# Kernel tuning notes

Measured on AMD Instinct MI355X. Metric: run time of the kernel, lower is better.

## Reference

```python
import jax, jax.numpy as jnp
import numpy as np

B, N, D = 4, 2048, 512   # batch, seq, feed_forward_size
H, DK, DV = 8, 64, 64    # heads, key_dim, value_dim
LN_EPS = 1e-5


def setup_inputs() -> dict:
    key = jax.random.key(0)
    ks = jax.random.split(key, 12)
    s = 0.02
    x = jax.random.normal(ks[0], (B, N, D), dtype=jnp.float32)
    # boolean mask, True = masked out (torch masked_fill semantics); causal
    attn_mask = ~jnp.tril(jnp.ones((N, N), dtype=bool))[None, None]
    ln_g = jnp.ones((D,), jnp.float32)
    ln_b = jnp.zeros((D,), jnp.float32)
    wq = jax.random.normal(ks[1], (D, H * DK), jnp.float32) * s
    bq = jnp.zeros((H * DK,), jnp.float32)
    wk = jax.random.normal(ks[2], (D, H * DK), jnp.float32) * s
    bk = jnp.zeros((H * DK,), jnp.float32)
    wv = jax.random.normal(ks[3], (D, H * DV), jnp.float32) * s
    bv = jnp.zeros((H * DV,), jnp.float32)
    wo = jax.random.normal(ks[4], (H * DV, D), jnp.float32) * s
    bo = jnp.zeros((D,), jnp.float32)
    return {"x": x, "attn_mask": attn_mask, "ln_g": ln_g, "ln_b": ln_b,
            "wq": wq, "bq": bq, "wk": wk, "bk": bk, "wv": wv, "bv": bv,
            "wo": wo, "bo": bo}


def _layernorm(x, g, b):
    mu = jnp.mean(x, axis=-1, keepdims=True)
    var = jnp.mean(jnp.square(x - mu), axis=-1, keepdims=True)
    return (x - mu) * jax.lax.rsqrt(var + LN_EPS) * g + b


def reference(x, attn_mask, ln_g, ln_b, wq, bq, wk, bk, wv, bv, wo, bo):
    xn = _layernorm(x, ln_g, ln_b)
    scale = DK ** -0.5
    q = (xn @ wq + bq).reshape(B, N, H, DK).transpose(0, 2, 1, 3) * scale  # b h n d
    k = (xn @ wk + bk).reshape(B, N, H, DK).transpose(0, 2, 1, 3)
    v = (xn @ wv + bv).reshape(B, N, H, DV).transpose(0, 2, 1, 3)
    sim = jnp.einsum('bhid,bhjd->bhij', q, k)
    sim = jnp.where(attn_mask, -jnp.finfo(sim.dtype).max, sim)
    attn = jax.nn.softmax(sim, axis=-1)  # dropout p=0 (eval)
    out = jnp.einsum('bhij,bhjd->bhid', attn, v)
    out = out.transpose(0, 2, 1, 3).reshape(B, N, H * DV)  # b n (h d)
    return out @ wo + bo
```

## Files before the change

kernel.cpp:

```cpp
#include <hip/hip_runtime.h>

typedef unsigned short u16;
typedef unsigned long long u64;
typedef __bf16 bf16x8 __attribute__((ext_vector_type(8)));
typedef float f32x4 __attribute__((ext_vector_type(4)));
typedef float f32x16 __attribute__((ext_vector_type(16)));

#define H_HEADS 8
#define DHEAD 64
#define NSEQ 2048
#define DMODEL 512
#define BATCH 4
#define MROWS (BATCH * NSEQ)
#define BH (BATCH * H_HEADS)

__device__ __forceinline__ u16 f2bf(float f) {
  unsigned u = __builtin_bit_cast(unsigned, f);
  u += 0x7fffu + ((u >> 16) & 1u);
  return (u16)(u >> 16);
}

__device__ __forceinline__ bf16x8 ldfrag(const u16* p) {
  return __builtin_bit_cast(bf16x8, *(const uint4*)p);
}

typedef __attribute__((address_space(1))) void GV;
typedef __attribute__((address_space(3))) void LV;
__device__ __forceinline__ void gld16(const void* g, void* l) {
  __builtin_amdgcn_global_load_lds((GV*)g, (LV*)l, 16, 0, 0);
}

__global__ __launch_bounds__(256) void ln_kernel(
    const float* __restrict__ x, const float* __restrict__ g,
    const float* __restrict__ b, u16* __restrict__ xn) {
  const int row = blockIdx.x;
  const int t = threadIdx.x;
  const float2 v = *(const float2*)(x + (size_t)row * DMODEL + t * 2);
  float s = v.x + v.y;
  float ss = v.x * v.x + v.y * v.y;
  #pragma unroll
  for (int d = 1; d < 64; d <<= 1) {
    s += __shfl_xor(s, d);
    ss += __shfl_xor(ss, d);
  }
  __shared__ float red[8];
  const int wave = t >> 6, lane = t & 63;
  if (lane == 0) { red[wave] = s; red[4 + wave] = ss; }
  __syncthreads();
  s = red[0] + red[1] + red[2] + red[3];
  ss = red[4] + red[5] + red[6] + red[7];
  const float mean = s * (1.0f / DMODEL);
  const float var = ss * (1.0f / DMODEL) - mean * mean;
  const float rstd = rsqrtf(var + 1e-5f);
  const float2 gg = *(const float2*)(g + t * 2);
  const float2 bb = *(const float2*)(b + t * 2);
  const float o0 = (v.x - mean) * rstd * gg.x + bb.x;
  const float o1 = (v.y - mean) * rstd * gg.y + bb.y;
  const unsigned packed = (unsigned)f2bf(o0) | ((unsigned)f2bf(o1) << 16);
  *(unsigned*)(xn + (size_t)row * DMODEL + t * 2) = packed;
}

__global__ __launch_bounds__(256) void transpose_w4_kernel(
    const float* __restrict__ w0, const float* __restrict__ w1,
    const float* __restrict__ w2, const float* __restrict__ w3,
    u16* __restrict__ WT) {
  __shared__ float tile[32][33];
  const int z = blockIdx.z;
  const float* W = (z == 0) ? w0 : (z == 1) ? w1 : (z == 2) ? w2 : w3;
  u16* dst = WT + (size_t)z * DMODEL * DMODEL;
  const int n0 = blockIdx.x * 32, k0 = blockIdx.y * 32;
  const int t = threadIdx.x;
  #pragma unroll
  for (int p = 0; p < 4; ++p) {
    const int u = p * 256 + t;
    const int r = u >> 5, c = u & 31;
    tile[r][c] = W[(size_t)(k0 + r) * DMODEL + n0 + c];
  }
  __syncthreads();
  #pragma unroll
  for (int p = 0; p < 4; ++p) {
    const int u = p * 256 + t;
    const int rn = u >> 5, ck = u & 31;
    dst[(size_t)(n0 + rn) * DMODEL + k0 + ck] = f2bf(tile[ck][rn]);
  }
}

template <int MODE>
__global__ __launch_bounds__(512) void gemm128_kernel(
    const u16* __restrict__ A, const u16* __restrict__ BT,
    const float* __restrict__ bq, const float* __restrict__ bk,
    const float* __restrict__ bv,
    u16* __restrict__ qb, u16* __restrict__ kb, u16* __restrict__ vtb,
    float* __restrict__ fout, int K) {
  __shared__ u16 lds_a[128 * 64];
  __shared__ u16 lds_b[128 * 64];
  const int t = threadIdx.x;
  const int lane = t & 63, wave = t >> 6;
  const int wm = wave >> 2, wn = wave & 3;
  const int lo = lane & 15, hi = lane >> 4;
  const int nwg = gridDim.x * gridDim.y;
  const int lid = blockIdx.y * gridDim.x + blockIdx.x;
  const int sid = (lid & 7) * (nwg >> 3) + (lid >> 3);
  const int m0 = (sid / gridDim.x) * 128, n0 = (sid % gridDim.x) * 128;
  const int sr = lane >> 3;
  const int scol = (((lane & 7) ^ sr) * 8);
  f32x4 acc[4][2] = {};
  for (int k0 = 0; k0 < K; k0 += 64) {
    #pragma unroll
    for (int j = 0; j < 2; ++j) {
      const int ch = wave * 2 + j;
      gld16(A + (size_t)(m0 + ch * 8 + sr) * K + k0 + scol, lds_a + ch * 512);
      gld16(BT + (size_t)(n0 + ch * 8 + sr) * K + k0 + scol, lds_b + ch * 512);
    }
    __syncthreads();
    #pragma unroll
    for (int kc = 0; kc < 2; ++kc) {
      bf16x8 af[4], bfr[2];
      const int sw = ((lo & 7) * 8);
      #pragma unroll
      for (int i = 0; i < 4; ++i)
        af[i] = ldfrag(lds_a + (wm * 64 + i * 16 + lo) * 64 + ((kc * 32 + hi * 8) ^ sw));
      #pragma unroll
      for (int i = 0; i < 2; ++i)
        bfr[i] = ldfrag(lds_b + (wn * 32 + i * 16 + lo) * 64 + ((kc * 32 + hi * 8) ^ sw));
      __builtin_amdgcn_s_setprio(1);
      #pragma unroll
      for (int mi = 0; mi < 4; ++mi)
        #pragma unroll
        for (int ni = 0; ni < 2; ++ni)
          acc[mi][ni] = __builtin_amdgcn_mfma_f32_16x16x32_bf16(
              af[mi], bfr[ni], acc[mi][ni], 0, 0, 0);
      __builtin_amdgcn_s_setprio(0);
    }
    __syncthreads();
  }
  #pragma unroll
  for (int mi = 0; mi < 4; ++mi) {
    #pragma unroll
    for (int ni = 0; ni < 2; ++ni) {
      const int col = n0 + wn * 32 + ni * 16 + lo;
      if (MODE == 0) {
        const int mat = col >> 9, w = col & 511;
        const int hh = w >> 6, dk = w & 63;
        const float bi = (mat == 0 ? bq : (mat == 1 ? bk : bv))[w];
        const int row0 = m0 + wm * 64 + mi * 16 + hi * 4;
        const int bbx = row0 >> 11, seq0 = row0 & 2047;
        if (mat == 2) {
          u64 pk = 0;
          #pragma unroll
          for (int r = 0; r < 4; ++r)
            pk |= (u64)f2bf(acc[mi][ni][r] + bi) << (16 * r);
          *(u64*)(vtb + ((size_t)(bbx * H_HEADS + hh) * DHEAD + dk) * NSEQ + seq0) = pk;
        } else {
          const float sc = (mat == 0) ? 0.18033688f : 1.0f;
          u16* dst = (mat == 0 ? qb : kb);
          #pragma unroll
          for (int r = 0; r < 4; ++r)
            dst[(((size_t)(bbx * H_HEADS + hh) * NSEQ) + seq0 + r) * DHEAD + dk] =
                f2bf((acc[mi][ni][r] + bi) * sc);
        }
      } else {
        const float bi = bq[col];
        #pragma unroll
        for (int r = 0; r < 4; ++r) {
          const int row = m0 + wm * 64 + mi * 16 + hi * 4 + r;
          fout[(size_t)row * DMODEL + col] = acc[mi][ni][r] + bi;
        }
      }
    }
  }
}

__global__ __launch_bounds__(256, 4) void attn_kernel(
    const u16* __restrict__ Q, const u16* __restrict__ K,
    const u16* __restrict__ VT, u16* __restrict__ O,
    float* __restrict__ pO, float* __restrict__ pML) {
  __shared__ u16 lds_k[2][4096];
  __shared__ u16 lds_v[2][4096];
  const int t = threadIdx.x;
  const int lane = t & 63, wave = t >> 6;
  const int l31 = lane & 31, hi = lane >> 5;
  const int l7 = lane & 7;

  const int nraw = blockIdx.x;
  const int n = (nraw & 7) * 160 + (nraw >> 3);
  const int bh = n / 40;
  const int r = n % 40;
  int qt, ck, C;
  if (r < 4)       { qt = r;                 C = 1; ck = 0; }
  else if (r < 12) { qt = 4 + ((r - 4) >> 1);  C = 2; ck = (r - 4) & 1; }
  else if (r < 24) { qt = 8 + (r - 12) / 3;    C = 3; ck = (r - 12) % 3; }
  else             { qt = 12 + ((r - 24) >> 2); C = 4; ck = (r - 24) & 3; }
  const int T = 2 * qt + 2;
  const int kc0 = ck * 8;
  const int L = min(8, T - kc0);

  const int b = bh >> 3, h = bh & 7;
  const u16* Qh = Q + (size_t)bh * NSEQ * DHEAD;
  const u16* Kh = K + (size_t)bh * NSEQ * DHEAD;
  const u16* Vh = VT + (size_t)bh * DHEAD * NSEQ;

  const int q0w = qt * 128 + wave * 32;
  const int lastkt = (q0w + 31) >> 6;
  const int qrow = q0w + l31;

  bf16x8 qf[4];
  #pragma unroll
  for (int c = 0; c < 4; ++c)
    qf[c] = ldfrag(Qh + (size_t)qrow * DHEAD + c * 16 + hi * 8);

  f32x16 o0 = {}, o1 = {};
  float m = -INFINITY, l = 0.0f;

  const int sr = lane >> 3;
  const int scol = ((lane & 7) ^ sr) * 8;
  const int swz = l7 * 8;

  #pragma unroll
  for (int j = 0; j < 2; ++j) {
    const int ch = wave * 2 + j;
    gld16(Kh + (size_t)(kc0 * 64 + ch * 8 + sr) * DHEAD + scol, lds_k[0] + ch * 512);
    gld16(Vh + (size_t)(ch * 8 + sr) * NSEQ + kc0 * 64 + scol, lds_v[0] + ch * 512);
  }

  for (int lt = 0; lt < L; ++lt) {
    const int gk = kc0 + lt;
    const int cur = lt & 1;
    if (lt + 1 < L) {
      const int kvn = (gk + 1) * 64;
      #pragma unroll
      for (int j = 0; j < 2; ++j) {
        const int ch = wave * 2 + j;
        gld16(Kh + (size_t)(kvn + ch * 8 + sr) * DHEAD + scol, lds_k[cur ^ 1] + ch * 512);
        gld16(Vh + (size_t)(ch * 8 + sr) * NSEQ + kvn + scol, lds_v[cur ^ 1] + ch * 512);
      }
      asm volatile("s_waitcnt vmcnt(4)" ::: "memory");
    } else {
      asm volatile("s_waitcnt vmcnt(0)" ::: "memory");
    }
    __builtin_amdgcn_s_barrier();
    __builtin_amdgcn_sched_barrier(0);

    if (gk <= lastkt) {
      const u16* lk = lds_k[cur];
      const u16* lv = lds_v[cur];
      f32x16 st0 = {}, st1 = {};

      __builtin_amdgcn_s_setprio(1);
      #pragma unroll
      for (int c = 0; c < 4; ++c) {
        const int col = (c * 16 + hi * 8) ^ swz;
        bf16x8 kf0 = ldfrag(lk + l31 * 64 + col);
        bf16x8 kf1 = ldfrag(lk + (32 + l31) * 64 + col);
        st0 = __builtin_amdgcn_mfma_f32_32x32x16_bf16(kf0, qf[c], st0, 0, 0, 0);
        st1 = __builtin_amdgcn_mfma_f32_32x32x16_bf16(kf1, qf[c], st1, 0, 0, 0);
      }
      __builtin_amdgcn_s_setprio(0);

      if (gk == lastkt) {
        const int kvb = gk * 64 + 4 * hi;
        #pragma unroll
        for (int rr = 0; rr < 16; ++rr) {
          const int kv = kvb + (rr & 3) + 8 * (rr >> 2);
          if (kv > qrow) st0[rr] = -1e30f;
          if (kv + 32 > qrow) st1[rr] = -1e30f;
        }
      }

      float mx[16];
      #pragma unroll
      for (int i = 0; i < 16; ++i) mx[i] = fmaxf(st0[i], st1[i]);
      #pragma unroll
      for (int stp = 8; stp; stp >>= 1)
        #pragma unroll
        for (int i = 0; i < stp; ++i) mx[i] = fmaxf(mx[i], mx[i + stp]);
      float pm = fmaxf(mx[0], __shfl_xor(mx[0], 32));

      if (__any(pm > m + 8.0f)) {
        const float mn = fmaxf(m, pm);
        const float sc = exp2f(m - mn);
        m = mn;
        l *= sc;
        #pragma unroll
        for (int rr = 0; rr < 16; ++rr) { o0[rr] *= sc; o1[rr] *= sc; }
      }

      #pragma unroll
      for (int rr = 0; rr < 16; ++rr) st0[rr] = exp2f(st0[rr] - m);
      #pragma unroll
      for (int rr = 0; rr < 16; ++rr) st1[rr] = exp2f(st1[rr] - m);
      float sm[16];
      #pragma unroll
      for (int i = 0; i < 16; ++i) sm[i] = st0[i] + st1[i];
      #pragma unroll
      for (int stp = 8; stp; stp >>= 1)
        #pragma unroll
        for (int i = 0; i < stp; ++i) sm[i] += sm[i + stp];
      l += sm[0] + __shfl_xor(sm[0], 32);

      bf16x8 pf0, pf1, pf2, pf3;
      {
        unsigned w0, w1, w2, w3, w4, w5, w6, w7;
        asm("v_cvt_pk_bf16_f32 %0, %1, %2" : "=v"(w0) : "v"(st0[0]), "v"(st0[1]));
        asm("v_cvt_pk_bf16_f32 %0, %1, %2" : "=v"(w1) : "v"(st0[2]), "v"(st0[3]));
        asm("v_cvt_pk_bf16_f32 %0, %1, %2" : "=v"(w2) : "v"(st0[4]), "v"(st0[5]));
        asm("v_cvt_pk_bf16_f32 %0, %1, %2" : "=v"(w3) : "v"(st0[6]), "v"(st0[7]));
        asm("v_cvt_pk_bf16_f32 %0, %1, %2" : "=v"(w4) : "v"(st0[8]), "v"(st0[9]));
        asm("v_cvt_pk_bf16_f32 %0, %1, %2" : "=v"(w5) : "v"(st0[10]), "v"(st0[11]));
        asm("v_cvt_pk_bf16_f32 %0, %1, %2" : "=v"(w6) : "v"(st0[12]), "v"(st0[13]));
        asm("v_cvt_pk_bf16_f32 %0, %1, %2" : "=v"(w7) : "v"(st0[14]), "v"(st0[15]));
        asm("v_permlane32_swap_b32 %0, %1" : "+v"(w0), "+v"(w2));
        asm("v_permlane32_swap_b32 %0, %1" : "+v"(w1), "+v"(w3));
        asm("v_permlane32_swap_b32 %0, %1" : "+v"(w4), "+v"(w6));
        asm("v_permlane32_swap_b32 %0, %1" : "+v"(w5), "+v"(w7));
        union Uu { unsigned u[4]; bf16x8 v; };
        Uu a; a.u[0] = w0; a.u[1] = w1; a.u[2] = w2; a.u[3] = w3; pf0 = a.v;
        Uu bb; bb.u[0] = w4; bb.u[1] = w5; bb.u[2] = w6; bb.u[3] = w7; pf1 = bb.v;
      }
      {
        unsigned w0, w1, w2, w3, w4, w5, w6, w7;
        asm("v_cvt_pk_bf16_f32 %0, %1, %2" : "=v"(w0) : "v"(st1[0]), "v"(st1[1]));
        asm("v_cvt_pk_bf16_f32 %0, %1, %2" : "=v"(w1) : "v"(st1[2]), "v"(st1[3]));
        asm("v_cvt_pk_bf16_f32 %0, %1, %2" : "=v"(w2) : "v"(st1[4]), "v"(st1[5]));
        asm("v_cvt_pk_bf16_f32 %0, %1, %2" : "=v"(w3) : "v"(st1[6]), "v"(st1[7]));
        asm("v_cvt_pk_bf16_f32 %0, %1, %2" : "=v"(w4) : "v"(st1[8]), "v"(st1[9]));
        asm("v_cvt_pk_bf16_f32 %0, %1, %2" : "=v"(w5) : "v"(st1[10]), "v"(st1[11]));
        asm("v_cvt_pk_bf16_f32 %0, %1, %2" : "=v"(w6) : "v"(st1[12]), "v"(st1[13]));
        asm("v_cvt_pk_bf16_f32 %0, %1, %2" : "=v"(w7) : "v"(st1[14]), "v"(st1[15]));
        asm("v_permlane32_swap_b32 %0, %1" : "+v"(w0), "+v"(w2));
        asm("v_permlane32_swap_b32 %0, %1" : "+v"(w1), "+v"(w3));
        asm("v_permlane32_swap_b32 %0, %1" : "+v"(w4), "+v"(w6));
        asm("v_permlane32_swap_b32 %0, %1" : "+v"(w5), "+v"(w7));
        union Uu { unsigned u[4]; bf16x8 v; };
        Uu a; a.u[0] = w0; a.u[1] = w1; a.u[2] = w2; a.u[3] = w3; pf2 = a.v;
        Uu bb; bb.u[0] = w4; bb.u[1] = w5; bb.u[2] = w6; bb.u[3] = w7; pf3 = bb.v;
      }

      __builtin_amdgcn_s_setprio(1);
      #pragma unroll
      for (int c = 0; c < 4; ++c) {
        const int col = (c * 16 + hi * 8) ^ swz;
        bf16x8 vf0 = ldfrag(lv + l31 * 64 + col);
        bf16x8 vf1 = ldfrag(lv + (32 + l31) * 64 + col);
        const bf16x8 pc = (c == 0) ? pf0 : (c == 1) ? pf1 : (c == 2) ? pf2 : pf3;
        o0 = __builtin_amdgcn_mfma_f32_32x32x16_bf16(vf0, pc, o0, 0, 0, 0);
        o1 = __builtin_amdgcn_mfma_f32_32x32x16_bf16(vf1, pc, o1, 0, 0, 0);
      }
      __builtin_amdgcn_s_setprio(0);
    }
    __builtin_amdgcn_sched_barrier(0);
    __builtin_amdgcn_s_barrier();
    __builtin_amdgcn_sched_barrier(0);
  }

  if (C == 1) {
    const float rl = __builtin_amdgcn_rcpf(l);
    u16* Ob = O + ((size_t)b * NSEQ + qrow) * DMODEL + h * DHEAD;
    #pragma unroll
    for (int d = 0; d < 2; ++d) {
      #pragma unroll
      for (int mq = 0; mq < 4; ++mq) {
        u64 pk = 0;
        #pragma unroll
        for (int c3 = 0; c3 < 4; ++c3) {
          const float v = (d ? o1[mq * 4 + c3] : o0[mq * 4 + c3]) * rl;
          pk |= (u64)f2bf(v) << (16 * c3);
        }
        *(u64*)(Ob + d * 32 + mq * 8 + hi * 4) = pk;
      }
    }
  } else {
    const int rloc = wave * 32 + l31;
    float* po = pO + (size_t)n * (128 * 64) + (size_t)rloc * 64;
    #pragma unroll
    for (int mq = 0; mq < 4; ++mq) {
      f32x4 v0 = {o0[mq * 4], o0[mq * 4 + 1], o0[mq * 4 + 2], o0[mq * 4 + 3]};
      *(f32x4*)(po + mq * 8 + hi * 4) = v0;
      f32x4 v1 = {o1[mq * 4], o1[mq * 4 + 1], o1[mq * 4 + 2], o1[mq * 4 + 3]};
      *(f32x4*)(po + 32 + mq * 8 + hi * 4) = v1;
    }
    if (hi == 0) {
      pML[(size_t)n * 256 + rloc] = m;
      pML[(size_t)n * 256 + 128 + rloc] = l;
    }
  }
}

__global__ __launch_bounds__(256) void attn_merge_kernel(
    const float* __restrict__ pO, const float* __restrict__ pML,
    u16* __restrict__ O) {
  const int u = blockIdx.x;
  const int bh = u / 12, qi = u % 12;
  const int qt = 4 + qi;
  const int C = (qt >> 2) + 1;
  int off;
  if (qt < 8) off = 4 + 2 * (qt - 4);
  else if (qt < 12) off = 12 + 3 * (qt - 8);
  else off = 24 + 4 * (qt - 12);
  const int slot0 = bh * 40 + off;
  const int t = threadIdx.x;
  const int row = t >> 1, db = (t & 1) * 32;

  float mc[4], lc[4];
  #pragma unroll
  for (int c = 0; c < 4; ++c) {
    if (c < C) {
      mc[c] = pML[(size_t)(slot0 + c) * 256 + row];
      lc[c] = pML[(size_t)(slot0 + c) * 256 + 128 + row];
    } else { mc[c] = -INFINITY; lc[c] = 0.0f; }
  }
  float ms = fmaxf(fmaxf(mc[0], mc[1]), fmaxf(mc[2], mc[3]));
  float w[4], ls = 0.0f;
  #pragma unroll
  for (int c = 0; c < 4; ++c) {
    w[c] = (c < C) ? exp2f(mc[c] - ms) : 0.0f;
    ls += w[c] * lc[c];
  }
  const float rl = __builtin_amdgcn_rcpf(ls);

  f32x4 a[8] = {};
  #pragma unroll
  for (int c = 0; c < 4; ++c) {
    if (c < C) {
      const float* src = pO + (size_t)(slot0 + c) * (128 * 64) + (size_t)row * 64 + db;
      const float wc = w[c];
      #pragma unroll
      for (int k = 0; k < 8; ++k) {
        const f32x4 v = *(const f32x4*)(src + k * 4);
        a[k] += v * wc;
      }
    }
  }
  const int b = bh >> 3, h = bh & 7;
  u16* dst = O + ((size_t)b * NSEQ + qt * 128 + row) * DMODEL + h * DHEAD + db;
  #pragma unroll
  for (int k = 0; k < 8; k += 1) {
    u64 pk = 0;
    #pragma unroll
    for (int j = 0; j < 4; ++j)
      pk |= (u64)f2bf(a[k][j] * rl) << (16 * j);
    *(u64*)(dst + k * 4) = pk;
  }
}

extern "C" void kernel_launch(void* const* d_in, const int* in_sizes, int n_in,
                              void* d_out, int out_size, void* d_ws, size_t ws_size,
                              hipStream_t stream) {
  const float* x = (const float*)d_in[0];
  const float* ln_g = (const float*)d_in[2];
  const float* ln_b = (const float*)d_in[3];
  const float* wq = (const float*)d_in[4];
  const float* bq = (const float*)d_in[5];
  const float* wk = (const float*)d_in[6];
  const float* bk = (const float*)d_in[7];
  const float* wv = (const float*)d_in[8];
  const float* bv = (const float*)d_in[9];
  const float* wo = (const float*)d_in[10];
  const float* bo = (const float*)d_in[11];

  char* ws = (char*)d_ws;
  u16* xn = (u16*)ws;     ws += (size_t)MROWS * DMODEL * 2;
  u16* wqkvT = (u16*)ws;  ws += (size_t)4 * DMODEL * DMODEL * 2;
  u16* woT = wqkvT + (size_t)3 * DMODEL * DMODEL;
  u16* qb = (u16*)ws;     ws += (size_t)MROWS * DMODEL * 2;
  u16* kb = (u16*)ws;     ws += (size_t)MROWS * DMODEL * 2;
  u16* vtb = (u16*)ws;    ws += (size_t)MROWS * DMODEL * 2;
  u16* attnb = (u16*)ws;  ws += (size_t)MROWS * DMODEL * 2;
  float* pO = (float*)ws; ws += (size_t)1280 * 128 * 64 * 4;
  float* pML = (float*)ws; ws += (size_t)1280 * 256 * 4;

  ln_kernel<<<MROWS, 256, 0, stream>>>(x, ln_g, ln_b, xn);
  transpose_w4_kernel<<<dim3(16, 16, 4), 256, 0, stream>>>(wq, wk, wv, wo, wqkvT);

  gemm128_kernel<0><<<dim3(12, 64), 512, 0, stream>>>(
      xn, wqkvT, bq, bk, bv, qb, kb, vtb, nullptr, DMODEL);

  attn_kernel<<<1280, 256, 0, stream>>>(qb, kb, vtb, attnb, pO, pML);
  attn_merge_kernel<<<384, 256, 0, stream>>>(pO, pML, attnb);

  gemm128_kernel<1><<<dim3(4, 64), 512, 0, stream>>>(
      attnb, woT, bo, nullptr, nullptr, nullptr, nullptr, nullptr,
      (float*)d_out, DMODEL);
}
```

Baseline: 108.4 us.

## Shrink attention KV tile to 32, rebalance split-K chunks, store partials in bf16

The attention kernel now iterates over 32-row KV tiles instead of 64, with halved LDS buffers and a new V swizzle. Occupancy is raised to 6 blocks per SM and the causal work split is redone as 72 chunks per head, up to 8 tiles each. Partial outputs are stored as bf16 rather than fp32 to cut merge traffic, and the merge kernel loops over a variable chunk count. This trades more loop iterations, barriers and softmax rescale checks for better load balance and occupancy, at some precision cost in the partials.

```diff
diff --git a/kernel.cpp b/kernel.cpp
--- a/kernel.cpp
+++ b/kernel.cpp
@@ -13,11 +13,18 @@
 #define BATCH 4
 #define MROWS (BATCH * NSEQ)
 #define BH (BATCH * H_HEADS)
+#define NCHUNK 72
+#define NBLK (BH * NCHUNK)
 
 __device__ __forceinline__ u16 f2bf(float f) {
   unsigned u = __builtin_bit_cast(unsigned, f);
   u += 0x7fffu + ((u >> 16) & 1u);
   return (u16)(u >> 16);
+}
+
+__device__ __forceinline__ float bf2f(u16 v) {
+  unsigned u = (unsigned)v << 16;
+  return __builtin_bit_cast(float, u);
 }
 
 __device__ __forceinline__ bf16x8 ldfrag(const u16* p) {
@@ -171,27 +178,27 @@
   }
 }
 
-__global__ __launch_bounds__(256, 4) void attn_kernel(
+__global__ __launch_bounds__(256, 6) void attn_kernel(
     const u16* __restrict__ Q, const u16* __restrict__ K,
     const u16* __restrict__ VT, u16* __restrict__ O,
-    float* __restrict__ pO, float* __restrict__ pML) {
-  __shared__ u16 lds_k[2][4096];
-  __shared__ u16 lds_v[2][4096];
+    u16* __restrict__ pO, float* __restrict__ pML) {
+  __shared__ u16 lds_k[2][2048];
+  __shared__ u16 lds_v[2][2048];
   const int t = threadIdx.x;
   const int lane = t & 63, wave = t >> 6;
   const int l31 = lane & 31, hi = lane >> 5;
-  const int l7 = lane & 7;
 
   const int nraw = blockIdx.x;
-  const int n = (nraw & 7) * 160 + (nraw >> 3);
-  const int bh = n / 40;
-  const int r = n % 40;
-  int qt, ck, C;
-  if (r < 4)       { qt = r;                 C = 1; ck = 0; }
-  else if (r < 12) { qt = 4 + ((r - 4) >> 1);  C = 2; ck = (r - 4) & 1; }
-  else if (r < 24) { qt = 8 + (r - 12) / 3;    C = 3; ck = (r - 12) % 3; }
-  else             { qt = 12 + ((r - 24) >> 2); C = 4; ck = (r - 24) & 3; }
-  const int T = 2 * qt + 2;
+  const int n = (nraw & 7) * (NBLK / 8) + (nraw >> 3);
+  const int bh = n / NCHUNK;
+  const int r = n % NCHUNK;
+  int qt = 0, off = 0, C = 1, ck = 0;
+  while (true) {
+    C = (qt + 2) >> 1;
+    if (r < off + C) { ck = r - off; break; }
+    off += C; ++qt;
+  }
+  const int T = 4 * qt + 4;
   const int kc0 = ck * 8;
   const int L = min(8, T - kc0);
 
@@ -201,7 +208,7 @@
   const u16* Vh = VT + (size_t)bh * DHEAD * NSEQ;
 
   const int q0w = qt * 128 + wave * 32;
-  const int lastkt = (q0w + 31) >> 6;
+  const int lastkt = (q0w + 31) >> 5;
   const int qrow = q0w + l31;
 
   bf16x8 qf[4];
@@ -212,29 +219,28 @@
   f32x16 o0 = {}, o1 = {};
   float m = -INFINITY, l = 0.0f;
 
-  const int sr = lane >> 3;
-  const int scol = ((lane & 7) ^ sr) * 8;
-  const int swz = l7 * 8;
-
-  #pragma unroll
-  for (int j = 0; j < 2; ++j) {
-    const int ch = wave * 2 + j;
-    gld16(Kh + (size_t)(kc0 * 64 + ch * 8 + sr) * DHEAD + scol, lds_k[0] + ch * 512);
-    gld16(Vh + (size_t)(ch * 8 + sr) * NSEQ + kc0 * 64 + scol, lds_v[0] + ch * 512);
+  const int srk = lane >> 3;
+  const int sck = ((lane & 7) ^ srk) * 8;
+  const int dvs = wave * 16 + (lane >> 2);
+  const int vsw_s = ((dvs >> 1) ^ (dvs >> 3)) & 3;
+  const int scv = ((lane & 3) ^ vsw_s) * 8;
+  const int vsw = ((l31 >> 1) ^ (l31 >> 3)) & 3;
+  const int ksw = (l31 & 7) * 8;
+
+  #pragma unroll
+  for (int j = 0; j < 1; ++j) {
+    gld16(Kh + (size_t)(kc0 * 32 + wave * 8 + srk) * DHEAD + sck, lds_k[0] + wave * 512);
+    gld16(Vh + (size_t)dvs * NSEQ + kc0 * 32 + scv, lds_v[0] + wave * 512);
   }
 
   for (int lt = 0; lt < L; ++lt) {
     const int gk = kc0 + lt;
     const int cur = lt & 1;
     if (lt + 1 < L) {
-      const int kvn = (gk + 1) * 64;
-      #pragma unroll
-      for (int j = 0; j < 2; ++j) {
-        const int ch = wave * 2 + j;
-        gld16(Kh + (size_t)(kvn + ch * 8 + sr) * DHEAD + scol, lds_k[cur ^ 1] + ch * 512);
-        gld16(Vh + (size_t)(ch * 8 + sr) * NSEQ + kvn + scol, lds_v[cur ^ 1] + ch * 512);
-      }
-      asm volatile("s_waitcnt vmcnt(4)" ::: "memory");
+      const int kvn = (gk + 1) * 32;
+      gld16(Kh + (size_t)(kvn + wave * 8 + srk) * DHEAD + sck, lds_k[cur ^ 1] + wave * 512);
+      gld16(Vh + (size_t)dvs * NSEQ + kvn + scv, lds_v[cur ^ 1] + wave * 512);
+      asm volatile("s_waitcnt vmcnt(2)" ::: "memory");
     } else {
       asm volatile("s_waitcnt vmcnt(0)" ::: "memory");
     }
@@ -244,34 +250,30 @@
     if (gk <= lastkt) {
       const u16* lk = lds_k[cur];
       const u16* lv = lds_v[cur];
-      f32x16 st0 = {}, st1 = {};
+      f32x16 st0 = {};
 
       __builtin_amdgcn_s_setprio(1);
       #pragma unroll
       for (int c = 0; c < 4; ++c) {
-        const int col = (c * 16 + hi * 8) ^ swz;
-        bf16x8 kf0 = ldfrag(lk + l31 * 64 + col);
-        bf16x8 kf1 = ldfrag(lk + (32 + l31) * 64 + col);
-        st0 = __builtin_amdgcn_mfma_f32_32x32x16_bf16(kf0, qf[c], st0, 0, 0, 0);
-        st1 = __builtin_amdgcn_mfma_f32_32x32x16_bf16(kf1, qf[c], st1, 0, 0, 0);
+        bf16x8 kf = ldfrag(lk + l31 * 64 + ((c * 16 + hi * 8) ^ ksw));
+        st0 = __builtin_amdgcn_mfma_f32_32x32x16_bf16(kf, qf[c], st0, 0, 0, 0);
       }
       __builtin_amdgcn_s_setprio(0);
 
       if (gk == lastkt) {
-        const int kvb = gk * 64 + 4 * hi;
+        const int kvb = gk * 32 + 4 * hi;
         #pragma unroll
         for (int rr = 0; rr < 16; ++rr) {
           const int kv = kvb + (rr & 3) + 8 * (rr >> 2);
           if (kv > qrow) st0[rr] = -1e30f;
-          if (kv + 32 > qrow) st1[rr] = -1e30f;
         }
       }
 
-      float mx[16];
-      #pragma unroll
-      for (int i = 0; i < 16; ++i) mx[i] = fmaxf(st0[i], st1[i]);
-      #pragma unroll
-      for (int stp = 8; stp; stp >>= 1)
+      float mx[8];
+      #pragma unroll
+      for (int i = 0; i < 8; ++i) mx[i] = fmaxf(st0[i], st0[i + 8]);
+      #pragma unroll
+      for (int stp = 4; stp; stp >>= 1)
         #pragma unroll
         for (int i = 0; i < stp; ++i) mx[i] = fmaxf(mx[i], mx[i + stp]);
       float pm = fmaxf(mx[0], __shfl_xor(mx[0], 32));
@@ -287,18 +289,16 @@
 
       #pragma unroll
       for (int rr = 0; rr < 16; ++rr) st0[rr] = exp2f(st0[rr] - m);
-      #pragma unroll
-      for (int rr = 0; rr < 16; ++rr) st1[rr] = exp2f(st1[rr] - m);
-      float sm[16];
-      #pragma unroll
-      for (int i = 0; i < 16; ++i) sm[i] = st0[i] + st1[i];
-      #pragma unroll
-      for (int stp = 8; stp; stp >>= 1)
+      float sm[8];
+      #pragma unroll
+      for (int i = 0; i < 8; ++i) sm[i] = st0[i] + st0[i + 8];
+      #pragma unroll
+      for (int stp = 4; stp; stp >>= 1)
         #pragma unroll
         for (int i = 0; i < stp; ++i) sm[i] += sm[i + stp];
       l += sm[0] + __shfl_xor(sm[0], 32);
 
-      bf16x8 pf0, pf1, pf2, pf3;
+      bf16x8 pf0, pf1;
       {
         unsigned w0, w1, w2, w3, w4, w5, w6, w7;
         asm("v_cvt_pk_bf16_f32 %0, %1, %2" : "=v"(w0) : "v"(st0[0]), "v"(st0[1]));
@@ -317,32 +317,14 @@
         Uu a; a.u[0] = w0; a.u[1] = w1; a.u[2] = w2; a.u[3] = w3; pf0 = a.v;
         Uu bb; bb.u[0] = w4; bb.u[1] = w5; bb.u[2] = w6; bb.u[3] = w7; pf1 = bb.v;
       }
-      {
-        unsigned w0, w1, w2, w3, w4, w5, w6, w7;
-        asm("v_cvt_pk_bf16_f32 %0, %1, %2" : "=v"(w0) : "v"(st1[0]), "v"(st1[1]));
-        asm("v_cvt_pk_bf16_f32 %0, %1, %2" : "=v"(w1) : "v"(st1[2]), "v"(st1[3]));
-        asm("v_cvt_pk_bf16_f32 %0, %1, %2" : "=v"(w2) : "v"(st1[4]), "v"(st1[5]));
-        asm("v_cvt_pk_bf16_f32 %0, %1, %2" : "=v"(w3) : "v"(st1[6]), "v"(st1[7]));
-        asm("v_cvt_pk_bf16_f32 %0, %1, %2" : "=v"(w4) : "v"(st1[8]), "v"(st1[9]));
-        asm("v_cvt_pk_bf16_f32 %0, %1, %2" : "=v"(w5) : "v"(st1[10]), "v"(st1[11]));
-        asm("v_cvt_pk_bf16_f32 %0, %1, %2" : "=v"(w6) : "v"(st1[12]), "v"(st1[13]));
-        asm("v_cvt_pk_bf16_f32 %0, %1, %2" : "=v"(w7) : "v"(st1[14]), "v"(st1[15]));
-        asm("v_permlane32_swap_b32 %0, %1" : "+v"(w0), "+v"(w2));
-        asm("v_permlane32_swap_b32 %0, %1" : "+v"(w1), "+v"(w3));
-        asm("v_permlane32_swap_b32 %0, %1" : "+v"(w4), "+v"(w6));
-        asm("v_permlane32_swap_b32 %0, %1" : "+v"(w5), "+v"(w7));
-        union Uu { unsigned u[4]; bf16x8 v; };
-        Uu a; a.u[0] = w0; a.u[1] = w1; a.u[2] = w2; a.u[3] = w3; pf2 = a.v;
-        Uu bb; bb.u[0] = w4; bb.u[1] = w5; bb.u[2] = w6; bb.u[3] = w7; pf3 = bb.v;
-      }
 
       __builtin_amdgcn_s_setprio(1);
       #pragma unroll
-      for (int c = 0; c < 4; ++c) {
-        const int col = (c * 16 + hi * 8) ^ swz;
-        bf16x8 vf0 = ldfrag(lv + l31 * 64 + col);
-        bf16x8 vf1 = ldfrag(lv + (32 + l31) * 64 + col);
-        const bf16x8 pc = (c == 0) ? pf0 : (c == 1) ? pf1 : (c == 2) ? pf2 : pf3;
+      for (int c = 0; c < 2; ++c) {
+        const int slot = (c * 2 + hi) ^ vsw;
+        bf16x8 vf0 = ldfrag(lv + l31 * 32 + slot * 8);
+        bf16x8 vf1 = ldfrag(lv + (32 + l31) * 32 + slot * 8);
+        const bf16x8 pc = c ? pf1 : pf0;
         o0 = __builtin_amdgcn_mfma_f32_32x32x16_bf16(vf0, pc, o0, 0, 0, 0);
         o1 = __builtin_amdgcn_mfma_f32_32x32x16_bf16(vf1, pc, o1, 0, 0, 0);
       }
@@ -371,13 +353,19 @@
     }
   } else {
     const int rloc = wave * 32 + l31;
-    float* po = pO + (size_t)n * (128 * 64) + (size_t)rloc * 64;
-    #pragma unroll
-    for (int mq = 0; mq < 4; ++mq) {
-      f32x4 v0 = {o0[mq * 4], o0[mq * 4 + 1], o0[mq * 4 + 2], o0[mq * 4 + 3]};
-      *(f32x4*)(po + mq * 8 + hi * 4) = v0;
-      f32x4 v1 = {o1[mq * 4], o1[mq * 4 + 1], o1[mq * 4 + 2], o1[mq * 4 + 3]};
-      *(f32x4*)(po + 32 + mq * 8 + hi * 4) = v1;
+    u16* po = pO + (size_t)n * (128 * 64) + (size_t)rloc * 64;
+    #pragma unroll
+    for (int d = 0; d < 2; ++d) {
+      #pragma unroll
+      for (int mq = 0; mq < 4; ++mq) {
+        u64 pk = 0;
+        #pragma unroll
+        for (int c3 = 0; c3 < 4; ++c3) {
+          const float v = d ? o1[mq * 4 + c3] : o0[mq * 4 + c3];
+          pk |= (u64)f2bf(v) << (16 * c3);
+        }
+        *(u64*)(po + d * 32 + mq * 8 + hi * 4) = pk;
+      }
     }
     if (hi == 0) {
       pML[(size_t)n * 256 + rloc] = m;
@@ -387,59 +375,53 @@
 }
 
 __global__ __launch_bounds__(256) void attn_merge_kernel(
-    const float* __restrict__ pO, const float* __restrict__ pML,
+    const u16* __restrict__ pO, const float* __restrict__ pML,
     u16* __restrict__ O) {
   const int u = blockIdx.x;
-  const int bh = u / 12, qi = u % 12;
-  const int qt = 4 + qi;
-  const int C = (qt >> 2) + 1;
-  int off;
-  if (qt < 8) off = 4 + 2 * (qt - 4);
-  else if (qt < 12) off = 12 + 3 * (qt - 8);
-  else off = 24 + 4 * (qt - 12);
-  const int slot0 = bh * 40 + off;
+  const int bh = u / 14, qi = u % 14;
+  const int qt = 2 + qi;
+  const int C = (qt + 2) >> 1;
+  const int mm = qt >> 1;
+  const int off = (qt & 1) ? (mm + 1) * (mm + 1) : mm * (mm + 1);
+  const int slot0 = bh * NCHUNK + off;
   const int t = threadIdx.x;
   const int row = t >> 1, db = (t & 1) * 32;
 
-  float mc[4], lc[4];
-  #pragma unroll
-  for (int c = 0; c < 4; ++c) {
-    if (c < C) {
-      mc[c] = pML[(size_t)(slot0 + c) * 256 + row];
-      lc[c] = pML[(size_t)(slot0 + c) * 256 + 128 + row];
-    } else { mc[c] = -INFINITY; lc[c] = 0.0f; }
-  }
-  float ms = fmaxf(fmaxf(mc[0], mc[1]), fmaxf(mc[2], mc[3]));
-  float w[4], ls = 0.0f;
-  #pragma unroll
-  for (int c = 0; c < 4; ++c) {
-    w[c] = (c < C) ? exp2f(mc[c] - ms) : 0.0f;
-    ls += w[c] * lc[c];
+  float ms = -INFINITY;
+  for (int c = 0; c < C; ++c)
+    ms = fmaxf(ms, pML[(size_t)(slot0 + c) * 256 + row]);
+
+  float ls = 0.0f;
+  float a[32];
+  #pragma unroll
+  for (int k = 0; k < 32; ++k) a[k] = 0.0f;
+  for (int c = 0; c < C; ++c) {
+    const float mc = pML[(size_t)(slot0 + c) * 256 + row];
+    const float lc = pML[(size_t)(slot0 + c) * 256 + 128 + row];
+    const float wc = exp2f(mc - ms);
+    ls += wc * lc;
+    const u16* src = pO + (size_t)(slot0 + c) * (128 * 64) + (size_t)row * 64 + db;
+    #pragma unroll
+    for (int q4 = 0; q4 < 4; ++q4) {
+      const uint4 v = *(const uint4*)(src + q4 * 8);
+      const unsigned uu[4] = {v.x, v.y, v.z, v.w};
+      #pragma unroll
+      for (int j = 0; j < 4; ++j) {
+        a[q4 * 8 + j * 2]     += wc * bf2f((u16)(uu[j] & 0xffff));
+        a[q4 * 8 + j * 2 + 1] += wc * bf2f((u16)(uu[j] >> 16));
+      }
+    }
   }
   const float rl = __builtin_amdgcn_rcpf(ls);
-
-  f32x4 a[8] = {};
-  #pragma unroll
-  for (int c = 0; c < 4; ++c) {
-    if (c < C) {
-      const float* src = pO + (size_t)(slot0 + c) * (128 * 64) + (size_t)row * 64 + db;
-      const float wc = w[c];
-      #pragma unroll
-      for (int k = 0; k < 8; ++k) {
-        const f32x4 v = *(const f32x4*)(src + k * 4);
-        a[k] += v * wc;
-      }
-    }
-  }
   const int b = bh >> 3, h = bh & 7;
   u16* dst = O + ((size_t)b * NSEQ + qt * 128 + row) * DMODEL + h * DHEAD + db;
   #pragma unroll
-  for (int k = 0; k < 8; k += 1) {
+  for (int k4 = 0; k4 < 8; ++k4) {
     u64 pk = 0;
     #pragma unroll
     for (int j = 0; j < 4; ++j)
-      pk |= (u64)f2bf(a[k][j] * rl) << (16 * j);
-    *(u64*)(dst + k * 4) = pk;
+      pk |= (u64)f2bf(a[k4 * 4 + j] * rl) << (16 * j);
+    *(u64*)(dst + k4 * 4) = pk;
   }
 }
 
@@ -466,8 +448,8 @@
   u16* kb = (u16*)ws;     ws += (size_t)MROWS * DMODEL * 2;
   u16* vtb = (u16*)ws;    ws += (size_t)MROWS * DMODEL * 2;
   u16* attnb = (u16*)ws;  ws += (size_t)MROWS * DMODEL * 2;
-  float* pO = (float*)ws; ws += (size_t)1280 * 128 * 64 * 4;
-  float* pML = (float*)ws; ws += (size_t)1280 * 256 * 4;
+  u16* pO = (u16*)ws;     ws += (size_t)NBLK * 128 * 64 * 2;
+  float* pML = (float*)ws; ws += (size_t)NBLK * 256 * 4;
 
   ln_kernel<<<MROWS, 256, 0, stream>>>(x, ln_g, ln_b, xn);
   transpose_w4_kernel<<<dim3(16, 16, 4), 256, 0, stream>>>(wq, wk, wv, wo, wqkvT);
@@ -475,8 +457,8 @@
   gemm128_kernel<0><<<dim3(12, 64), 512, 0, stream>>>(
       xn, wqkvT, bq, bk, bv, qb, kb, vtb, nullptr, DMODEL);
 
-  attn_kernel<<<1280, 256, 0, stream>>>(qb, kb, vtb, attnb, pO, pML);
-  attn_merge_kernel<<<384, 256, 0, stream>>>(pO, pML, attnb);
+  attn_kernel<<<NBLK, 256, 0, stream>>>(qb, kb, vtb, attnb, pO, pML);
+  attn_merge_kernel<<<32 * 14, 256, 0, stream>>>(pO, pML, attnb);
 
   gemm128_kernel<1><<<dim3(4, 64), 512, 0, stream>>>(
       attnb, woT, bo, nullptr, nullptr, nullptr, nullptr, nullptr,
```

Result: slower. 139.4 us (+28.5%).

## Fuse layernorm with weight transpose, store split-K partials in bf16, balance chunks

Applied to the files above, without the earlier changes.

Merges the layernorm and weight-transpose kernels into one launch, using blockIdx to pick the role, which removes one kernel launch. Attention split-K partial outputs are now stored as bf16 instead of fp32, halving partial-output traffic in both the attention and merge kernels. Key-tile chunks are now divided evenly across the C splits instead of in fixed groups of 8, which balances work between blocks. Storing partials in bf16 adds rounding error before the merge.

```diff
diff --git a/kernel.cpp b/kernel.cpp
--- a/kernel.cpp
+++ b/kernel.cpp
@@ -20,6 +20,11 @@
   return (u16)(u >> 16);
 }
 
+__device__ __forceinline__ float bf2f(u16 v) {
+  unsigned u = (unsigned)v << 16;
+  return __builtin_bit_cast(float, u);
+}
+
 __device__ __forceinline__ bf16x8 ldfrag(const u16* p) {
   return __builtin_bit_cast(bf16x8, *(const uint4*)p);
 }
@@ -30,58 +35,58 @@
   __builtin_amdgcn_global_load_lds((GV*)g, (LV*)l, 16, 0, 0);
 }
 
-__global__ __launch_bounds__(256) void ln_kernel(
+__global__ __launch_bounds__(256) void ln_w_kernel(
     const float* __restrict__ x, const float* __restrict__ g,
-    const float* __restrict__ b, u16* __restrict__ xn) {
-  const int row = blockIdx.x;
-  const int t = threadIdx.x;
-  const float2 v = *(const float2*)(x + (size_t)row * DMODEL + t * 2);
-  float s = v.x + v.y;
-  float ss = v.x * v.x + v.y * v.y;
-  #pragma unroll
-  for (int d = 1; d < 64; d <<= 1) {
-    s += __shfl_xor(s, d);
-    ss += __shfl_xor(ss, d);
-  }
-  __shared__ float red[8];
-  const int wave = t >> 6, lane = t & 63;
-  if (lane == 0) { red[wave] = s; red[4 + wave] = ss; }
-  __syncthreads();
-  s = red[0] + red[1] + red[2] + red[3];
-  ss = red[4] + red[5] + red[6] + red[7];
-  const float mean = s * (1.0f / DMODEL);
-  const float var = ss * (1.0f / DMODEL) - mean * mean;
-  const float rstd = rsqrtf(var + 1e-5f);
-  const float2 gg = *(const float2*)(g + t * 2);
-  const float2 bb = *(const float2*)(b + t * 2);
-  const float o0 = (v.x - mean) * rstd * gg.x + bb.x;
-  const float o1 = (v.y - mean) * rstd * gg.y + bb.y;
-  const unsigned packed = (unsigned)f2bf(o0) | ((unsigned)f2bf(o1) << 16);
-  *(unsigned*)(xn + (size_t)row * DMODEL + t * 2) = packed;
-}
-
-__global__ __launch_bounds__(256) void transpose_w4_kernel(
+    const float* __restrict__ b, u16* __restrict__ xn,
     const float* __restrict__ w0, const float* __restrict__ w1,
     const float* __restrict__ w2, const float* __restrict__ w3,
     u16* __restrict__ WT) {
   __shared__ float tile[32][33];
-  const int z = blockIdx.z;
-  const float* W = (z == 0) ? w0 : (z == 1) ? w1 : (z == 2) ? w2 : w3;
-  u16* dst = WT + (size_t)z * DMODEL * DMODEL;
-  const int n0 = blockIdx.x * 32, k0 = blockIdx.y * 32;
   const int t = threadIdx.x;
-  #pragma unroll
-  for (int p = 0; p < 4; ++p) {
-    const int u = p * 256 + t;
-    const int r = u >> 5, c = u & 31;
-    tile[r][c] = W[(size_t)(k0 + r) * DMODEL + n0 + c];
-  }
-  __syncthreads();
-  #pragma unroll
-  for (int p = 0; p < 4; ++p) {
-    const int u = p * 256 + t;
-    const int rn = u >> 5, ck = u & 31;
-    dst[(size_t)(n0 + rn) * DMODEL + k0 + ck] = f2bf(tile[ck][rn]);
+  if (blockIdx.x < MROWS) {
+    const int row = blockIdx.x;
+    const float2 v = *(const float2*)(x + (size_t)row * DMODEL + t * 2);
+    float s = v.x + v.y;
+    float ss = v.x * v.x + v.y * v.y;
+    #pragma unroll
+    for (int d = 1; d < 64; d <<= 1) {
+      s += __shfl_xor(s, d);
+      ss += __shfl_xor(ss, d);
+    }
+    const int wave = t >> 6, lane = t & 63;
+    if (lane == 0) { tile[0][wave] = s; tile[0][4 + wave] = ss; }
+    __syncthreads();
+    s = tile[0][0] + tile[0][1] + tile[0][2] + tile[0][3];
+    ss = tile[0][4] + tile[0][5] + tile[0][6] + tile[0][7];
+    const float mean = s * (1.0f / DMODEL);
+    const float var = ss * (1.0f / DMODEL) - mean * mean;
+    const float rstd = rsqrtf(var + 1e-5f);
+    const float2 gg = *(const float2*)(g + t * 2);
+    const float2 bb = *(const float2*)(b + t * 2);
+    const float o0 = (v.x - mean) * rstd * gg.x + bb.x;
+    const float o1 = (v.y - mean) * rstd * gg.y + bb.y;
+    const unsigned packed = (unsigned)f2bf(o0) | ((unsigned)f2bf(o1) << 16);
+    *(unsigned*)(xn + (size_t)row * DMODEL + t * 2) = packed;
+  } else {
+    const int u = blockIdx.x - MROWS;
+    const int z = u >> 8;
+    const int rem = u & 255;
+    const float* W = (z == 0) ? w0 : (z == 1) ? w1 : (z == 2) ? w2 : w3;
+    u16* dst = WT + (size_t)z * DMODEL * DMODEL;
+    const int n0 = (rem & 15) * 32, k0 = (rem >> 4) * 32;
+    #pragma unroll
+    for (int p = 0; p < 4; ++p) {
+      const int uu = p * 256 + t;
+      const int r = uu >> 5, c = uu & 31;
+      tile[r][c] = W[(size_t)(k0 + r) * DMODEL + n0 + c];
+    }
+    __syncthreads();
+    #pragma unroll
+    for (int p = 0; p < 4; ++p) {
+      const int uu = p * 256 + t;
+      const int rn = uu >> 5, ck = uu & 31;
+      dst[(size_t)(n0 + rn) * DMODEL + k0 + ck] = f2bf(tile[ck][rn]);
+    }
   }
 }
 
@@ -174,7 +179,7 @@
 __global__ __launch_bounds__(256, 4) void attn_kernel(
     const u16* __restrict__ Q, const u16* __restrict__ K,
     const u16* __restrict__ VT, u16* __restrict__ O,
-    float* __restrict__ pO, float* __restrict__ pML) {
+    u16* __restrict__ pO, float* __restrict__ pML) {
   __shared__ u16 lds_k[2][4096];
   __shared__ u16 lds_v[2][4096];
   const int t = threadIdx.x;
@@ -192,8 +197,8 @@
   else if (r < 24) { qt = 8 + (r - 12) / 3;    C = 3; ck = (r - 12) % 3; }
   else             { qt = 12 + ((r - 24) >> 2); C = 4; ck = (r - 24) & 3; }
   const int T = 2 * qt + 2;
-  const int kc0 = ck * 8;
-  const int L = min(8, T - kc0);
+  const int kc0 = (ck * T) / C;
+  const int L = ((ck + 1) * T) / C - kc0;
 
   const int b = bh >> 3, h = bh & 7;
   const u16* Qh = Q + (size_t)bh * NSEQ * DHEAD;
@@ -371,13 +376,19 @@
     }
   } else {
     const int rloc = wave * 32 + l31;
-    float* po = pO + (size_t)n * (128 * 64) + (size_t)rloc * 64;
-    #pragma unroll
-    for (int mq = 0; mq < 4; ++mq) {
-      f32x4 v0 = {o0[mq * 4], o0[mq * 4 + 1], o0[mq * 4 + 2], o0[mq * 4 + 3]};
-      *(f32x4*)(po + mq * 8 + hi * 4) = v0;
-      f32x4 v1 = {o1[mq * 4], o1[mq * 4 + 1], o1[mq * 4 + 2], o1[mq * 4 + 3]};
-      *(f32x4*)(po + 32 + mq * 8 + hi * 4) = v1;
+    u16* po = pO + (size_t)n * (128 * 64) + (size_t)rloc * 64;
+    #pragma unroll
+    for (int d = 0; d < 2; ++d) {
+      #pragma unroll
+      for (int mq = 0; mq < 4; ++mq) {
+        u64 pk = 0;
+        #pragma unroll
+        for (int c3 = 0; c3 < 4; ++c3) {
+          const float v = d ? o1[mq * 4 + c3] : o0[mq * 4 + c3];
+          pk |= (u64)f2bf(v) << (16 * c3);
+        }
+        *(u64*)(po + d * 32 + mq * 8 + hi * 4) = pk;
+      }
     }
     if (hi == 0) {
       pML[(size_t)n * 256 + rloc] = m;
@@ -387,7 +398,7 @@
 }
 
 __global__ __launch_bounds__(256) void attn_merge_kernel(
-    const float* __restrict__ pO, const float* __restrict__ pML,
+    const u16* __restrict__ pO, const float* __restrict__ pML,
     u16* __restrict__ O) {
   const int u = blockIdx.x;
   const int bh = u / 12, qi = u % 12;
@@ -418,28 +429,35 @@
   }
   const float rl = __builtin_amdgcn_rcpf(ls);
 
-  f32x4 a[8] = {};
+  float a[32];
+  #pragma unroll
+  for (int k = 0; k < 32; ++k) a[k] = 0.0f;
   #pragma unroll
   for (int c = 0; c < 4; ++c) {
     if (c < C) {
-      const float* src = pO + (size_t)(slot0 + c) * (128 * 64) + (size_t)row * 64 + db;
+      const u16* src = pO + (size_t)(slot0 + c) * (128 * 64) + (size_t)row * 64 + db;
       const float wc = w[c];
       #pragma unroll
-      for (int k = 0; k < 8; ++k) {
-        const f32x4 v = *(const f32x4*)(src + k * 4);
-        a[k] += v * wc;
+      for (int q4 = 0; q4 < 4; ++q4) {
+        const uint4 v = *(const uint4*)(src + q4 * 8);
+        const unsigned uu[4] = {v.x, v.y, v.z, v.w};
+        #pragma unroll
+        for (int j = 0; j < 4; ++j) {
+          a[q4 * 8 + j * 2]     += wc * bf2f((u16)(uu[j] & 0xffff));
+          a[q4 * 8 + j * 2 + 1] += wc * bf2f((u16)(uu[j] >> 16));
+        }
       }
     }
   }
   const int b = bh >> 3, h = bh & 7;
   u16* dst = O + ((size_t)b * NSEQ + qt * 128 + row) * DMODEL + h * DHEAD + db;
   #pragma unroll
-  for (int k = 0; k < 8; k += 1) {
+  for (int k4 = 0; k4 < 8; ++k4) {
     u64 pk = 0;
     #pragma unroll
     for (int j = 0; j < 4; ++j)
-      pk |= (u64)f2bf(a[k][j] * rl) << (16 * j);
-    *(u64*)(dst + k * 4) = pk;
+      pk |= (u64)f2bf(a[k4 * 4 + j] * rl) << (16 * j);
+    *(u64*)(dst + k4 * 4) = pk;
   }
 }
 
@@ -466,11 +484,11 @@
   u16* kb = (u16*)ws;     ws += (size_t)MROWS * DMODEL * 2;
   u16* vtb = (u16*)ws;    ws += (size_t)MROWS * DMODEL * 2;
   u16* attnb = (u16*)ws;  ws += (size_t)MROWS * DMODEL * 2;
-  float* pO = (float*)ws; ws += (size_t)1280 * 128 * 64 * 4;
+  u16* pO = (u16*)ws;     ws += (size_t)1280 * 128 * 64 * 2;
   float* pML = (float*)ws; ws += (size_t)1280 * 256 * 4;
 
-  ln_kernel<<<MROWS, 256, 0, stream>>>(x, ln_g, ln_b, xn);
-  transpose_w4_kernel<<<dim3(16, 16, 4), 256, 0, stream>>>(wq, wk, wv, wo, wqkvT);
+  ln_w_kernel<<<MROWS + 1024, 256, 0, stream>>>(
+      x, ln_g, ln_b, xn, wq, wk, wv, wo, wqkvT);
 
   gemm128_kernel<0><<<dim3(12, 64), 512, 0, stream>>>(
       xn, wqkvT, bq, bk, bv, qb, kb, vtb, nullptr, DMODEL);
```

After: 100.6 us. 1.08x faster.
